# Kernel optimization log

Hardware: AMD Instinct MI355X
Metric: run time of the kernel (lower is better)

Reference implementation:

```python
import jax, jax.numpy as jnp
import numpy as np

N_HID, N_HEAD, N_K, N_V = 1024, 16, 64, 64
B, S = 2, 2048


def setup_inputs() -> dict:
    key = jax.random.key(0)
    ks = jax.random.split(key, 5)
    w_scale = 1.0 / np.sqrt(N_HID)  # keep pre-softmax logits in a sane range
    x = jax.random.normal(ks[0], (B, S, N_HID), dtype=jnp.float32)
    mask = jax.random.randint(ks[1], (B, S, N_HEAD, S), 0, 2) > 0  # [B, Sq, H, Sk] bool
    W_qkv = jax.random.normal(ks[2], (N_HID, N_HEAD * (2 * N_K + N_V)), dtype=jnp.float32) * w_scale
    b_qkv = jnp.zeros((N_HEAD * (2 * N_K + N_V),), dtype=jnp.float32)
    W_out = jax.random.normal(ks[3], (N_HEAD * N_V, N_HID), dtype=jnp.float32) * w_scale
    b_out = jnp.zeros((N_HID,), dtype=jnp.float32)
    return {"x": x, "mask": mask, "W_qkv": W_qkv, "b_qkv": b_qkv, "W_out": W_out, "b_out": b_out}


def reference(x, mask, W_qkv, b_qkv, W_out, b_out):
    nb, sl, nh = x.shape
    qkv = x @ W_qkv + b_qkv                                  # [B, S, H*(2k+v)]
    qkv = qkv.reshape(nb, sl, N_HEAD, 2 * N_K + N_V).transpose(0, 2, 1, 3)  # [B, H, S, 2k+v]
    q, k, v = qkv[..., :N_K], qkv[..., N_K:2 * N_K], qkv[..., 2 * N_K:]
    qk = jnp.einsum('bhqd,bhkd->bhqk', q, k) / np.sqrt(N_K)  # [B, H, Sq, Sk]
    # original masks on the [B, Sq, H, Sk] view; swap mask axes instead of qk
    mask_bhqk = jnp.swapaxes(mask, 1, 2)                     # [B, H, Sq, Sk]
    qk = jnp.where(mask_bhqk, qk, -jnp.inf)
    attn = jax.nn.softmax(qk, axis=-1)
    ctx = jnp.einsum('bhqk,bhkd->bhqd', attn, v)             # [B, H, S, n_v]
    ctx = ctx.transpose(0, 2, 1, 3).reshape(nb, sl, N_HEAD * N_V)
    out = ctx @ W_out + b_out
    return x + out
```

## Files before the change

kernel.cpp:

```cpp
#include <hip/hip_runtime.h>

#define SEQ 2048
#define NHEAD 16
#define NHID 1024

typedef __attribute__((ext_vector_type(8))) short bf16x8;
typedef __attribute__((ext_vector_type(4))) float f32x4;
typedef unsigned short u16;

__device__ inline u16 f2bf(float f) {
    union { float f; unsigned u; } v; v.f = f;
    unsigned r = v.u + 0x7FFFu + ((v.u >> 16) & 1u);
    return (u16)(r >> 16);
}

typedef __attribute__((address_space(3))) unsigned int  lds_uint;
typedef const __attribute__((address_space(1))) unsigned int glob_uint;
__device__ __forceinline__ void gl2lds16(const void* g, void* l) {
    __builtin_amdgcn_global_load_lds((glob_uint*)(unsigned long long)g,
                                     (lds_uint*)(unsigned int)(unsigned long long)l,
                                     16, 0, 0);
}

__global__ void cast_kernel(const float* __restrict__ in, u16* __restrict__ out, int n4) {
    int i = blockIdx.x * 256 + threadIdx.x;
    if (i < n4) {
        float4 v = ((const float4*)in)[i];
        ushort4 o;
        o.x = f2bf(v.x); o.y = f2bf(v.y); o.z = f2bf(v.z); o.w = f2bf(v.w);
        ((ushort4*)out)[i] = o;
    }
}

__global__ void transpose_cast(const float* __restrict__ in, u16* __restrict__ out, int R, int C) {
    __shared__ float tile[32][33];
    int bx = blockIdx.x * 32, by = blockIdx.y * 32;
    int tx = threadIdx.x & 31, ty = threadIdx.x >> 5;
#pragma unroll
    for (int i = ty; i < 32; i += 8) tile[i][tx] = in[(size_t)(by + i) * C + bx + tx];
    __syncthreads();
#pragma unroll
    for (int i = ty; i < 32; i += 8) out[(size_t)(bx + i) * R + by + tx] = f2bf(tile[tx][i]);
}

__launch_bounds__(256, 2)
__global__ void gemm_qkv(const u16* __restrict__ A, const u16* __restrict__ Bt,
                         const float* __restrict__ bias,
                         u16* __restrict__ qs, u16* __restrict__ ks, u16* __restrict__ vt) {
    __shared__ __align__(16) u16 Alds[128 * 64];
    __shared__ __align__(16) u16 Blds[128 * 64];
    const int tid = threadIdx.x;
    const int m0 = blockIdx.y * 128, n0 = blockIdx.x * 128;
    const int lane = tid & 63, wid = tid >> 6;
    const int wm = (wid & 1) * 64, wn = (wid >> 1) * 64;
    const int col = lane & 15, quad = lane >> 4;
    const int sr = tid >> 3, scg = (tid & 7) * 8;
    f32x4 acc[4][4] = {};
    for (int k0 = 0; k0 < 1024; k0 += 64) {
#pragma unroll
        for (int p = 0; p < 4; p++) {
            int r = sr + p * 32;
            gl2lds16(&A[(size_t)(m0 + r) * 1024 + k0 + scg], &Alds[(p * 32 + wid * 8) * 64]);
            gl2lds16(&Bt[(size_t)(n0 + r) * 1024 + k0 + scg], &Blds[(p * 32 + wid * 8) * 64]);
        }
        __syncthreads();
#pragma unroll
        for (int kc = 0; kc < 2; kc++) {
            bf16x8 af[4], bfr[4];
#pragma unroll
            for (int t = 0; t < 4; t++) {
                af[t]  = *(const bf16x8*)&Alds[(wm + t * 16 + col) * 64 + kc * 32 + quad * 8];
                bfr[t] = *(const bf16x8*)&Blds[(wn + t * 16 + col) * 64 + kc * 32 + quad * 8];
            }
#pragma unroll
            for (int mt = 0; mt < 4; mt++)
#pragma unroll
                for (int nt = 0; nt < 4; nt++)
                    acc[mt][nt] = __builtin_amdgcn_mfma_f32_16x16x32_bf16(af[mt], bfr[nt], acc[mt][nt], 0, 0, 0);
        }
        __syncthreads();
    }
#pragma unroll
    for (int mt = 0; mt < 4; mt++)
#pragma unroll
        for (int nt = 0; nt < 4; nt++)
#pragma unroll
            for (int r = 0; r < 4; r++) {
                int gm = m0 + wm + mt * 16 + quad * 4 + r;
                int gn = n0 + wn + nt * 16 + col;
                float val = acc[mt][nt][r] + bias[gn];
                int b = gm >> 11, s = gm & 2047;
                int h = gn / 192, rr = gn - h * 192;
                size_t bh = (size_t)(b * NHEAD + h);
                if (rr < 64)       qs[(bh * SEQ + s) * 64 + rr] = f2bf(val * 0.125f);
                else if (rr < 128) ks[(bh * SEQ + s) * 64 + rr - 64] = f2bf(val);
                else               vt[(bh * 64 + rr - 128) * SEQ + s] = f2bf(val);
            }
}

__launch_bounds__(256, 2)
__global__ void attn_kernel(const u16* __restrict__ qs, const u16* __restrict__ ks,
                            const u16* __restrict__ vt, const int* __restrict__ mask,
                            u16* __restrict__ ctx) {
    __shared__ __align__(16) u16 Plds[4][16 * 72];
    const int tid = threadIdx.x;
    const int lane = tid & 63, wid = tid >> 6;
    const int col = lane & 15, quad = lane >> 4;
    const int bh = blockIdx.y, b = bh >> 4, h = bh & 15;
    const int q0 = blockIdx.x * 64 + wid * 16;
    const size_t hbase = (size_t)bh * SEQ * 64;

    const u16* qp = qs + hbase + (size_t)(q0 + col) * 64 + quad * 8;
    bf16x8 aq0 = *(const bf16x8*)qp;
    bf16x8 aq1 = *(const bf16x8*)(qp + 32);

    const int* mp[4];
#pragma unroll
    for (int r = 0; r < 4; r++)
        mp[r] = mask + (((size_t)b * SEQ + (q0 + quad * 4 + r)) * NHEAD + h) * SEQ + col;

    const u16* kbase = ks + hbase + (size_t)col * 64 + quad * 8;
    const u16* vbase = vt + ((size_t)bh * 64 + col) * SEQ + quad * 8;

    float m_i[4], l_i[4], alpha[4];
    f32x4 O[4] = {};
#pragma unroll
    for (int r = 0; r < 4; r++) { m_i[r] = -INFINITY; l_i[r] = 0.f; }

    for (int kb = 0; kb < SEQ; kb += 64) {
        f32x4 sacc[4];
#pragma unroll
        for (int nt = 0; nt < 4; nt++) {
            bf16x8 b0 = *(const bf16x8*)(kbase + (size_t)(kb + nt * 16) * 64);
            bf16x8 b1 = *(const bf16x8*)(kbase + (size_t)(kb + nt * 16) * 64 + 32);
            f32x4 z = {};
            z = __builtin_amdgcn_mfma_f32_16x16x32_bf16(aq0, b0, z, 0, 0, 0);
            z = __builtin_amdgcn_mfma_f32_16x16x32_bf16(aq1, b1, z, 0, 0, 0);
            sacc[nt] = z;
        }
        float sv[4][4];
#pragma unroll
        for (int nt = 0; nt < 4; nt++)
#pragma unroll
            for (int r = 0; r < 4; r++)
                sv[nt][r] = mp[r][kb + nt * 16] ? sacc[nt][r] : -1e30f;
#pragma unroll
        for (int r = 0; r < 4; r++) {
            float rm = fmaxf(fmaxf(sv[0][r], sv[1][r]), fmaxf(sv[2][r], sv[3][r]));
            rm = fmaxf(rm, __shfl_xor(rm, 1));
            rm = fmaxf(rm, __shfl_xor(rm, 2));
            rm = fmaxf(rm, __shfl_xor(rm, 4));
            rm = fmaxf(rm, __shfl_xor(rm, 8));
            float mnew = fmaxf(m_i[r], rm);
            alpha[r] = __expf(m_i[r] - mnew);
            m_i[r] = mnew;
        }
        float rsum[4] = {0.f, 0.f, 0.f, 0.f};
#pragma unroll
        for (int nt = 0; nt < 4; nt++)
#pragma unroll
            for (int r = 0; r < 4; r++) {
                float p = __expf(sv[nt][r] - m_i[r]);
                rsum[r] += p;
                Plds[wid][(quad * 4 + r) * 72 + nt * 16 + col] = f2bf(p);
            }
#pragma unroll
        for (int r = 0; r < 4; r++) {
            float rs = rsum[r];
            rs += __shfl_xor(rs, 1);
            rs += __shfl_xor(rs, 2);
            rs += __shfl_xor(rs, 4);
            rs += __shfl_xor(rs, 8);
            l_i[r] = l_i[r] * alpha[r] + rs;
        }
#pragma unroll
        for (int dt = 0; dt < 4; dt++)
#pragma unroll
            for (int r = 0; r < 4; r++) O[dt][r] *= alpha[r];

        bf16x8 ap0 = *(const bf16x8*)&Plds[wid][col * 72 + quad * 8];
        bf16x8 ap1 = *(const bf16x8*)&Plds[wid][col * 72 + 32 + quad * 8];
#pragma unroll
        for (int dt = 0; dt < 4; dt++) {
            bf16x8 bv0 = *(const bf16x8*)(vbase + (size_t)(dt * 16) * SEQ + kb);
            bf16x8 bv1 = *(const bf16x8*)(vbase + (size_t)(dt * 16) * SEQ + kb + 32);
            O[dt] = __builtin_amdgcn_mfma_f32_16x16x32_bf16(ap0, bv0, O[dt], 0, 0, 0);
            O[dt] = __builtin_amdgcn_mfma_f32_16x16x32_bf16(ap1, bv1, O[dt], 0, 0, 0);
        }
    }
#pragma unroll
    for (int dt = 0; dt < 4; dt++)
#pragma unroll
        for (int r = 0; r < 4; r++) {
            float val = O[dt][r] / l_i[r];
            int q = q0 + quad * 4 + r;
            ctx[(size_t)(b * SEQ + q) * NHID + h * 64 + dt * 16 + col] = f2bf(val);
        }
}

__launch_bounds__(256, 2)
__global__ void gemm_out(const u16* __restrict__ A, const u16* __restrict__ Bt,
                         const float* __restrict__ bias, const float* __restrict__ xres,
                         float* __restrict__ out) {
    __shared__ __align__(16) u16 Alds[128 * 64];
    __shared__ __align__(16) u16 Blds[128 * 64];
    const int tid = threadIdx.x;
    const int m0 = blockIdx.y * 128, n0 = blockIdx.x * 128;
    const int lane = tid & 63, wid = tid >> 6;
    const int wm = (wid & 1) * 64, wn = (wid >> 1) * 64;
    const int col = lane & 15, quad = lane >> 4;
    const int sr = tid >> 3, scg = (tid & 7) * 8;
    f32x4 acc[4][4] = {};
    for (int k0 = 0; k0 < 1024; k0 += 64) {
#pragma unroll
        for (int p = 0; p < 4; p++) {
            int r = sr + p * 32;
            gl2lds16(&A[(size_t)(m0 + r) * 1024 + k0 + scg], &Alds[(p * 32 + wid * 8) * 64]);
            gl2lds16(&Bt[(size_t)(n0 + r) * 1024 + k0 + scg], &Blds[(p * 32 + wid * 8) * 64]);
        }
        __syncthreads();
#pragma unroll
        for (int kc = 0; kc < 2; kc++) {
            bf16x8 af[4], bfr[4];
#pragma unroll
            for (int t = 0; t < 4; t++) {
                af[t]  = *(const bf16x8*)&Alds[(wm + t * 16 + col) * 64 + kc * 32 + quad * 8];
                bfr[t] = *(const bf16x8*)&Blds[(wn + t * 16 + col) * 64 + kc * 32 + quad * 8];
            }
#pragma unroll
            for (int mt = 0; mt < 4; mt++)
#pragma unroll
                for (int nt = 0; nt < 4; nt++)
                    acc[mt][nt] = __builtin_amdgcn_mfma_f32_16x16x32_bf16(af[mt], bfr[nt], acc[mt][nt], 0, 0, 0);
        }
        __syncthreads();
    }
#pragma unroll
    for (int mt = 0; mt < 4; mt++)
#pragma unroll
        for (int nt = 0; nt < 4; nt++)
#pragma unroll
            for (int r = 0; r < 4; r++) {
                int gm = m0 + wm + mt * 16 + quad * 4 + r;
                int gn = n0 + wn + nt * 16 + col;
                out[(size_t)gm * NHID + gn] = acc[mt][nt][r] + bias[gn] + xres[(size_t)gm * NHID + gn];
            }
}

extern "C" void kernel_launch(void* const* d_in, const int* in_sizes, int n_in,
                              void* d_out, int out_size, void* d_ws, size_t ws_size,
                              hipStream_t stream) {
    const float* x     = (const float*)d_in[0];
    const int*   mask  = (const int*)d_in[1];
    const float* W_qkv = (const float*)d_in[2];
    const float* b_qkv = (const float*)d_in[3];
    const float* W_out = (const float*)d_in[4];
    const float* b_out = (const float*)d_in[5];
    float* out = (float*)d_out;

    char* ws = (char*)d_ws;
    u16* x_bf   = (u16*)(ws);
    u16* wqkv_t = (u16*)(ws + (size_t)(8  << 20));
    u16* wout_t = (u16*)(ws + (size_t)(14 << 20));
    u16* qs     = (u16*)(ws + (size_t)(16 << 20));
    u16* ks     = (u16*)(ws + (size_t)(24 << 20));
    u16* vt     = (u16*)(ws + (size_t)(32 << 20));
    u16* ctx    = (u16*)(ws + (size_t)(40 << 20));

    cast_kernel<<<4096, 256, 0, stream>>>(x, x_bf, 4096 * 1024 / 4);
    transpose_cast<<<dim3(3072 / 32, 1024 / 32), 256, 0, stream>>>(W_qkv, wqkv_t, 1024, 3072);
    transpose_cast<<<dim3(1024 / 32, 1024 / 32), 256, 0, stream>>>(W_out, wout_t, 1024, 1024);
    gemm_qkv<<<dim3(24, 32), 256, 0, stream>>>(x_bf, wqkv_t, b_qkv, qs, ks, vt);
    attn_kernel<<<dim3(32, 32), 256, 0, stream>>>(qs, ks, vt, mask, ctx);
    gemm_out<<<dim3(8, 32), 256, 0, stream>>>(ctx, wout_t, b_out, x, out);
}
```

Before: 940.8 us.

## Stage K/V tiles through double-buffered LDS with async global-to-LDS loads

```diff
diff --git a/kernel.cpp b/kernel.cpp
--- a/kernel.cpp
+++ b/kernel.cpp
@@ -98,10 +98,12 @@
             }
 }
 
-__launch_bounds__(256, 2)
+__launch_bounds__(256, 3)
 __global__ void attn_kernel(const u16* __restrict__ qs, const u16* __restrict__ ks,
                             const u16* __restrict__ vt, const int* __restrict__ mask,
                             u16* __restrict__ ctx) {
+    __shared__ __align__(16) u16 Klds[2][64 * 64];
+    __shared__ __align__(16) u16 Vlds[2][64 * 64];
     __shared__ __align__(16) u16 Plds[4][16 * 72];
     const int tid = threadIdx.x;
     const int lane = tid & 63, wid = tid >> 6;
@@ -110,6 +112,8 @@
     const int q0 = blockIdx.x * 64 + wid * 16;
     const size_t hbase = (size_t)bh * SEQ * 64;
 
+    const int srow = lane >> 3, scol8 = (lane & 7) * 8;
+
     const u16* qp = qs + hbase + (size_t)(q0 + col) * 64 + quad * 8;
     bf16x8 aq0 = *(const bf16x8*)qp;
     bf16x8 aq1 = *(const bf16x8*)(qp + 32);
@@ -119,34 +123,54 @@
     for (int r = 0; r < 4; r++)
         mp[r] = mask + (((size_t)b * SEQ + (q0 + quad * 4 + r)) * NHEAD + h) * SEQ + col;
 
-    const u16* kbase = ks + hbase + (size_t)col * 64 + quad * 8;
-    const u16* vbase = vt + ((size_t)bh * 64 + col) * SEQ + quad * 8;
-
     float m_i[4], l_i[4], alpha[4];
     f32x4 O[4] = {};
 #pragma unroll
     for (int r = 0; r < 4; r++) { m_i[r] = -INFINITY; l_i[r] = 0.f; }
 
-    for (int kb = 0; kb < SEQ; kb += 64) {
+#pragma unroll
+    for (int p = 0; p < 2; p++) {
+        int rw = wid * 16 + p * 8;
+        gl2lds16(&ks[hbase + (size_t)(rw + srow) * 64 + scol8], &Klds[0][rw * 64]);
+        gl2lds16(&vt[((size_t)bh * 64 + rw + srow) * SEQ + scol8], &Vlds[0][rw * 64]);
+    }
+
+    for (int it = 0; it < 32; it++) {
+        const int cur = it & 1;
+        const int kb = it * 64;
+        __syncthreads();
+        if (it < 31) {
+#pragma unroll
+            for (int p = 0; p < 2; p++) {
+                int rw = wid * 16 + p * 8;
+                gl2lds16(&ks[hbase + (size_t)(kb + 64 + rw + srow) * 64 + scol8], &Klds[cur ^ 1][rw * 64]);
+                gl2lds16(&vt[((size_t)bh * 64 + rw + srow) * SEQ + kb + 64 + scol8], &Vlds[cur ^ 1][rw * 64]);
+            }
+        }
+        int mv[4][4];
+#pragma unroll
+        for (int nt = 0; nt < 4; nt++)
+#pragma unroll
+            for (int r = 0; r < 4; r++) mv[nt][r] = mp[r][kb + nt * 16];
+
         f32x4 sacc[4];
 #pragma unroll
         for (int nt = 0; nt < 4; nt++) {
-            bf16x8 b0 = *(const bf16x8*)(kbase + (size_t)(kb + nt * 16) * 64);
-            bf16x8 b1 = *(const bf16x8*)(kbase + (size_t)(kb + nt * 16) * 64 + 32);
+            bf16x8 b0 = *(const bf16x8*)&Klds[cur][(nt * 16 + col) * 64 + quad * 8];
+            bf16x8 b1 = *(const bf16x8*)&Klds[cur][(nt * 16 + col) * 64 + 32 + quad * 8];
             f32x4 z = {};
             z = __builtin_amdgcn_mfma_f32_16x16x32_bf16(aq0, b0, z, 0, 0, 0);
             z = __builtin_amdgcn_mfma_f32_16x16x32_bf16(aq1, b1, z, 0, 0, 0);
             sacc[nt] = z;
         }
-        float sv[4][4];
 #pragma unroll
         for (int nt = 0; nt < 4; nt++)
 #pragma unroll
             for (int r = 0; r < 4; r++)
-                sv[nt][r] = mp[r][kb + nt * 16] ? sacc[nt][r] : -1e30f;
+                if (!mv[nt][r]) sacc[nt][r] = -1e30f;
 #pragma unroll
         for (int r = 0; r < 4; r++) {
-            float rm = fmaxf(fmaxf(sv[0][r], sv[1][r]), fmaxf(sv[2][r], sv[3][r]));
+            float rm = fmaxf(fmaxf(sacc[0][r], sacc[1][r]), fmaxf(sacc[2][r], sacc[3][r]));
             rm = fmaxf(rm, __shfl_xor(rm, 1));
             rm = fmaxf(rm, __shfl_xor(rm, 2));
             rm = fmaxf(rm, __shfl_xor(rm, 4));
@@ -160,7 +184,7 @@
         for (int nt = 0; nt < 4; nt++)
 #pragma unroll
             for (int r = 0; r < 4; r++) {
-                float p = __expf(sv[nt][r] - m_i[r]);
+                float p = __expf(sacc[nt][r] - m_i[r]);
                 rsum[r] += p;
                 Plds[wid][(quad * 4 + r) * 72 + nt * 16 + col] = f2bf(p);
             }
@@ -182,17 +206,20 @@
         bf16x8 ap1 = *(const bf16x8*)&Plds[wid][col * 72 + 32 + quad * 8];
 #pragma unroll
         for (int dt = 0; dt < 4; dt++) {
-            bf16x8 bv0 = *(const bf16x8*)(vbase + (size_t)(dt * 16) * SEQ + kb);
-            bf16x8 bv1 = *(const bf16x8*)(vbase + (size_t)(dt * 16) * SEQ + kb + 32);
+            bf16x8 bv0 = *(const bf16x8*)&Vlds[cur][(dt * 16 + col) * 64 + quad * 8];
+            bf16x8 bv1 = *(const bf16x8*)&Vlds[cur][(dt * 16 + col) * 64 + 32 + quad * 8];
             O[dt] = __builtin_amdgcn_mfma_f32_16x16x32_bf16(ap0, bv0, O[dt], 0, 0, 0);
             O[dt] = __builtin_amdgcn_mfma_f32_16x16x32_bf16(ap1, bv1, O[dt], 0, 0, 0);
         }
     }
+    float rinv[4];
+#pragma unroll
+    for (int r = 0; r < 4; r++) rinv[r] = 1.f / l_i[r];
 #pragma unroll
     for (int dt = 0; dt < 4; dt++)
 #pragma unroll
         for (int r = 0; r < 4; r++) {
-            float val = O[dt][r] / l_i[r];
+            float val = O[dt][r] * rinv[r];
             int q = q0 + quad * 4 + r;
             ctx[(size_t)(b * SEQ + q) * NHID + h * 64 + dt * 16 + col] = f2bf(val);
         }
```

Result: faster. 850.1 us (-9.6%).
